# Performance work log

Hardware: AMD Instinct MI355X
Metric: run time of the kernel (lower is better)

## Reference

```python
import jax, jax.numpy as jnp
import numpy as np

B, S, D, H = 8, 512, 1024, 8
DPH = D // H            # 128, dim per head
MAX_REL = 32
NGRAM = 2               # 2-gram RNN on heads 4..7
NG_START, NG_COUNT = 4, 4
SCALE = float(DPH) ** 0.5


def setup_inputs() -> dict:
    key = jax.random.key(0)
    ks = jax.random.split(key, 12)
    w = lambda k, shp: jax.random.normal(k, shp, jnp.float32) * 0.02
    return {
        "x": jax.random.normal(ks[0], (B, S, D), jnp.float32),
        "mask": jax.random.randint(ks[1], (B, 1, S), 0, 2).astype(bool),
        "Wq": w(ks[2], (D, D)), "bq": jnp.zeros((D,), jnp.float32),
        "Wk": w(ks[3], (D, D)), "bk": jnp.zeros((D,), jnp.float32),
        "Wv": w(ks[4], (D, D)), "bv": jnp.zeros((D,), jnp.float32),
        "Wo": w(ks[5], (D, D)), "bo": jnp.zeros((D,), jnp.float32),
        "rel_emb": w(ks[6], (2 * MAX_REL + 1, DPH)),
        "Wih_f": w(ks[7], (DPH, DPH)), "Whh_f": w(ks[8], (DPH, DPH)),
        "bih_f": jnp.zeros((DPH,), jnp.float32), "bhh_f": jnp.zeros((DPH,), jnp.float32),
        "Wih_b": w(ks[9], (DPH, DPH)), "Whh_b": w(ks[10], (DPH, DPH)),
        "bih_b": jnp.zeros((DPH,), jnp.float32), "bhh_b": jnp.zeros((DPH,), jnp.float32),
    }


def reference(x, mask, Wq, bq, Wk, bk, Wv, bv, Wo, bo, rel_emb,
              Wih_f, Whh_f, bih_f, bhh_f, Wih_b, Whh_b, bih_b, bhh_b):
    shape_h = lambda t: t.reshape(B, S, H, DPH).transpose(0, 2, 1, 3)  # [B,H,S,d]
    q = shape_h(x @ Wq.T + bq)
    k = shape_h(x @ Wk.T + bk)
    v = shape_h(x @ Wv.T + bv)

    # --- ngram path: zero masked positions in q/k/v (all heads) ---
    m = mask[:, :, :, None]  # [B,1,S,1] broadcast over heads and d
    q = jnp.where(m, 0.0, q)
    k = jnp.where(m, 0.0, k)
    v = jnp.where(m, 0.0, v)

    # per-head 2-gram bidirectional RNN on heads NG_START..NG_START+NG_COUNT-1
    qh = q[:, NG_START:NG_START + NG_COUNT].reshape(-1, S, DPH)
    kh = k[:, NG_START:NG_START + NG_COUNT].reshape(-1, S, DPH)
    vh = v[:, NG_START:NG_START + NG_COUNT].reshape(-1, S, DPH)
    feats = jnp.concatenate([qh, kh, vh], axis=0)          # [3*B*NG_COUNT, S, d]
    shifted = jnp.pad(feats, ((0, 0), (1, 0), (0, 0)))[:, :-1]  # shift-by-1 (prev token)
    seq = jnp.stack([shifted, feats], axis=0).reshape(NGRAM, -1, DPH)  # [T, N*S, d]
    h0 = jnp.zeros((seq.shape[1], DPH), jnp.float32)
    fstep = lambda h, xt: (jnp.tanh(xt @ Wih_f.T + bih_f + h @ Whh_f.T + bhh_f), None)
    bstep = lambda h, xt: (jnp.tanh(xt @ Wih_b.T + bih_b + h @ Whh_b.T + bhh_b), None)
    hf, _ = jax.lax.scan(fstep, h0, seq)            # fwd final hidden
    hb, _ = jax.lax.scan(bstep, h0, seq[::-1])      # bwd final hidden
    yy = (hf + hb).reshape(3, B, NG_COUNT, S, DPH)  # sum of direction finals
    q = q.at[:, NG_START:NG_START + NG_COUNT].set(yy[0])
    k = k.at[:, NG_START:NG_START + NG_COUNT].set(yy[1])
    v = v.at[:, NG_START:NG_START + NG_COUNT].set(yy[2])

    # --- relative-position attention ---
    qs = q / SCALE
    r = jnp.arange(S)
    rel_idx = jnp.clip(r[None, :] - r[:, None], -MAX_REL, MAX_REL) + MAX_REL  # [S,S]
    rel_k = rel_emb[rel_idx]  # [S,S,d]; same table used for keys and values
    scores = jnp.einsum('bhqd,bhkd->bhqk', qs, k) + jnp.einsum('bhqd,qkd->bhqk', qs, rel_k)
    scores = jnp.where(mask[:, None], -1e18, scores)  # [B,1,1,S] broadcast
    attn = jax.nn.softmax(scores, axis=-1)
    ctx = jnp.einsum('bhqk,bhkd->bhqd', attn, v) + jnp.einsum('bhqk,qkd->bhqd', attn, rel_k)
    out = ctx.transpose(0, 2, 1, 3).reshape(B, S, D) @ Wo.T + bo
    return out, attn
```

## Files before the change

kernel.cpp:

```cpp
#include <hip/hip_runtime.h>


typedef __bf16 bf16x8 __attribute__((ext_vector_type(8)));
typedef float f32x4 __attribute__((ext_vector_type(4)));

#define MFMA16(a, b, c) __builtin_amdgcn_mfma_f32_16x16x32_bf16(a, b, c, 0, 0, 0)

__device__ __forceinline__ unsigned short f2bf(float f) {
  unsigned u = __float_as_uint(f);
  u += 0x7FFFu + ((u >> 16) & 1u);
  return (unsigned short)(u >> 16);
}
__device__ __forceinline__ uint2 pack4(float4 f) {
  uint2 r;
  r.x = (unsigned)f2bf(f.x) | ((unsigned)f2bf(f.y) << 16);
  r.y = (unsigned)f2bf(f.z) | ((unsigned)f2bf(f.w) << 16);
  return r;
}
__device__ __forceinline__ void gld16(const unsigned short* g, unsigned short* l) {
  __builtin_amdgcn_global_load_lds(
      (const __attribute__((address_space(1))) unsigned int*)g,
      (__attribute__((address_space(3))) unsigned int*)l, 16, 0, 0);
}

__global__ __launch_bounds__(256) void prep_bf16(
    const float* __restrict__ x,
    const float* __restrict__ Wq, const float* __restrict__ Wk,
    const float* __restrict__ Wv,
    const float* __restrict__ Wihf, const float* __restrict__ Whhf,
    const float* __restrict__ Wihb, const float* __restrict__ Whhb,
    unsigned short* __restrict__ xb, unsigned short* __restrict__ Wqkvb,
    unsigned short* __restrict__ Wrnnb) {
  int i = blockIdx.x * 256 + threadIdx.x;
  const float* src;
  unsigned short* dst;
  int off;
  if (i < 1048576) {
    src = x; dst = xb; off = i;
  } else if (i < 1310720) {
    src = Wq; dst = Wqkvb; off = i - 1048576;
  } else if (i < 1572864) {
    src = Wk; dst = Wqkvb + 1048576; off = i - 1310720;
  } else if (i < 1835008) {
    src = Wv; dst = Wqkvb + 2097152; off = i - 1572864;
  } else if (i < 1839104) {
    src = Wihf; dst = Wrnnb; off = i - 1835008;
  } else if (i < 1843200) {
    src = Whhf; dst = Wrnnb + 16384; off = i - 1839104;
  } else if (i < 1847296) {
    src = Wihb; dst = Wrnnb + 32768; off = i - 1843200;
  } else {
    src = Whhb; dst = Wrnnb + 49152; off = i - 1847296;
  }
  float4 f = *((const float4*)src + off);
  *(uint2*)(dst + (size_t)off * 4) = pack4(f);
}

__global__ __launch_bounds__(256) void qkv_proj(
    const unsigned short* __restrict__ xb, const unsigned short* __restrict__ Wqkvb,
    const float* __restrict__ bq, const float* __restrict__ bk,
    const float* __restrict__ bv, const int* __restrict__ mask,
    unsigned short* __restrict__ qb, unsigned short* __restrict__ kb,
    unsigned short* __restrict__ vb, unsigned short* __restrict__ vT) {
  __shared__ __align__(16) unsigned short As[128 * 64];
  __shared__ __align__(16) unsigned short Bs[128 * 64];
  const int bm = blockIdx.x & 31;
  const int bn = blockIdx.x >> 5;
  const int t = bn >> 3;
  const int nloc0 = (bn & 7) * 128;
  const unsigned short* W = Wqkvb + (size_t)t * 1048576;
  const float* bias = (t == 0) ? bq : (t == 1) ? bk : bv;
  const int tid = threadIdx.x;
  const int lane = tid & 63, w = tid >> 6;
  const int wm = (w >> 1) * 64, wn = (w & 1) * 64;
  const int lanelo = lane & 15, quad = lane >> 4;
  const int row0 = bm * 128;
  const int rloc = lane >> 3, pch = lane & 7;
  const int lch = (pch - rloc) & 7;

  f32x4 acc[4][4];
  const f32x4 zf = {0.f, 0.f, 0.f, 0.f};
#pragma unroll
  for (int i = 0; i < 4; ++i)
#pragma unroll
    for (int j = 0; j < 4; ++j) acc[i][j] = zf;

  for (int kt = 0; kt < 16; ++kt) {
#pragma unroll
    for (int q = 0; q < 4; ++q) {
      int seg = w * 4 + q;
      int grow = seg * 8 + rloc;
      gld16(xb + (size_t)(row0 + grow) * 1024 + kt * 64 + lch * 8, &As[seg * 512]);
      gld16(W + (size_t)(nloc0 + grow) * 1024 + kt * 64 + lch * 8, &Bs[seg * 512]);
    }
    __syncthreads();
#pragma unroll
    for (int ks = 0; ks < 2; ++ks) {
      const int pA = (ks * 4 + quad + lanelo) & 7;
      bf16x8 a[4], bb[4];
#pragma unroll
      for (int i = 0; i < 4; ++i)
        a[i] = *(const bf16x8*)(&As[(wm + i * 16 + lanelo) * 64 + pA * 8]);
#pragma unroll
      for (int j = 0; j < 4; ++j)
        bb[j] = *(const bf16x8*)(&Bs[(wn + j * 16 + lanelo) * 64 + pA * 8]);
#pragma unroll
      for (int i = 0; i < 4; ++i)
#pragma unroll
        for (int j = 0; j < 4; ++j) acc[i][j] = MFMA16(a[i], bb[j], acc[i][j]);
    }
    __syncthreads();
  }
#pragma unroll
  for (int i = 0; i < 4; ++i) {
#pragma unroll
    for (int j = 0; j < 4; ++j) {
      int jj = nloc0 + wn + j * 16 + lanelo;
      int hh = jj >> 7, dc = jj & 127;
      float bvv = bias[jj];
      int m0 = row0 + wm + i * 16 + quad * 4;
      int b0 = m0 >> 9, sS = m0 & 511;
      unsigned short ov[4];
#pragma unroll
      for (int r = 0; r < 4; ++r) {
        int s = sS + r;
        float val = acc[i][j][r] + bvv;
        if (mask[b0 * 512 + s]) val = 0.f;
        unsigned short o = f2bf(val);
        ov[r] = o;
        size_t off = ((size_t)(b0 * 8 + hh) * 512 + s) * 128 + dc;
        if (t == 0) qb[off] = o;
        else if (t == 1) kb[off] = o;
        else vb[off] = o;
      }
      if (t == 2) {
        uint2 pk;
        pk.x = (unsigned)ov[0] | ((unsigned)ov[1] << 16);
        pk.y = (unsigned)ov[2] | ((unsigned)ov[3] << 16);
        *(uint2*)(&vT[((size_t)(b0 * 8 + hh) * 128 + dc) * 512 + sS]) = pk;
      }
    }
  }
}

__global__ __launch_bounds__(256) void prep_rel(
    const float* __restrict__ rel, unsigned short* __restrict__ relb,
    unsigned short* __restrict__ relT) {
  int i = blockIdx.x * 256 + threadIdx.x;
  if (i < 65 * 128) relb[i] = f2bf(rel[i]);
  if (i < 128 * 96) {
    int d = i / 96, r = i - d * 96;
    relT[i] = (r < 65) ? f2bf(rel[r * 128 + d]) : (unsigned short)0;
  }
}

__global__ __launch_bounds__(256) void rnn_fused(
    const unsigned short* __restrict__ qb, const unsigned short* __restrict__ kb,
    const unsigned short* __restrict__ vb,
    const unsigned short* __restrict__ Wrnnb,
    const float* __restrict__ bihf, const float* __restrict__ bhhf,
    const float* __restrict__ bihb, const float* __restrict__ bhhb,
    unsigned short* __restrict__ rnn_out) {
  __shared__ __align__(16) unsigned short X[65 * 136];
  __shared__ __align__(16) unsigned short Wi[128 * 136];
  __shared__ __align__(16) unsigned short Wh[128 * 136];
  __shared__ __align__(16) unsigned short H1[64 * 136];
  __shared__ float cbf[128], cbb[128];

  const unsigned short* Wihfb = Wrnnb;
  const unsigned short* Whhfb = Wrnnb + 16384;
  const unsigned short* Wihbb = Wrnnb + 32768;
  const unsigned short* Whhbb = Wrnnb + 49152;

  const int gid = blockIdx.x;
  const int tile = gid & 7;
  const int g = gid >> 3;
  const int t = g >> 5;
  const int rem = g & 31;
  const int b = rem >> 2, h = (rem & 3) + 4;
  const int s0 = tile * 64;
  const unsigned short* src = (t == 0) ? qb : (t == 1) ? kb : vb;
  const size_t rowbase = (size_t)(b * 8 + h) * 512;
  const int tid = threadIdx.x;

  for (int c = tid; c < 65 * 16; c += 256) {
    int r = c >> 4, cc = c & 15;
    uint4 v4;
    if (r == 0 && s0 == 0) v4 = make_uint4(0, 0, 0, 0);
    else v4 = *(const uint4*)(src + (rowbase + (s0 - 1 + r)) * 128 + cc * 8);
    *(uint4*)(&X[r * 136 + cc * 8]) = v4;
  }
#pragma unroll
  for (int p = 0; p < 8; ++p) {
    int c = p * 256 + tid;
    int r = c >> 4, cc = c & 15;
    *(uint4*)(&Wi[r * 136 + cc * 8]) = *(const uint4*)(Wihfb + c * 8);
    *(uint4*)(&Wh[r * 136 + cc * 8]) = *(const uint4*)(Whhfb + c * 8);
  }
  if (tid < 128) {
    cbf[tid] = bihf[tid] + bhhf[tid];
    cbb[tid] = bihb[tid] + bhhb[tid];
  }
  __syncthreads();

  const int lane = tid & 63, w = tid >> 6;
  const int lanelo = lane & 15, quad = lane >> 4;
  const int marow = w * 16 + lanelo;
  const f32x4 zf = {0.f, 0.f, 0.f, 0.f};

  f32x4 g1[8];
#pragma unroll
  for (int j = 0; j < 8; ++j) g1[j] = zf;
#pragma unroll
  for (int ks = 0; ks < 4; ++ks) {
    bf16x8 a = *(const bf16x8*)(&X[marow * 136 + ks * 32 + quad * 8]);
#pragma unroll
    for (int j = 0; j < 8; ++j) {
      bf16x8 bb = *(const bf16x8*)(&Wi[(j * 16 + lanelo) * 136 + ks * 32 + quad * 8]);
      g1[j] = MFMA16(a, bb, g1[j]);
    }
  }
#pragma unroll
  for (int j = 0; j < 8; ++j) {
    int col = j * 16 + lanelo;
    float cb = cbf[col];
#pragma unroll
    for (int i = 0; i < 4; ++i) {
      int row = w * 16 + quad * 4 + i;
      H1[row * 136 + col] = f2bf(tanhf(g1[j][i] + cb));
    }
  }
  __syncthreads();
  f32x4 a2[8];
#pragma unroll
  for (int j = 0; j < 8; ++j) a2[j] = zf;
#pragma unroll
  for (int ks = 0; ks < 4; ++ks) {
    bf16x8 a = *(const bf16x8*)(&X[(marow + 1) * 136 + ks * 32 + quad * 8]);
#pragma unroll
    for (int j = 0; j < 8; ++j) {
      bf16x8 bb = *(const bf16x8*)(&Wi[(j * 16 + lanelo) * 136 + ks * 32 + quad * 8]);
      a2[j] = MFMA16(a, bb, a2[j]);
    }
  }
#pragma unroll
  for (int ks = 0; ks < 4; ++ks) {
    bf16x8 a = *(const bf16x8*)(&H1[marow * 136 + ks * 32 + quad * 8]);
#pragma unroll
    for (int j = 0; j < 8; ++j) {
      bf16x8 bb = *(const bf16x8*)(&Wh[(j * 16 + lanelo) * 136 + ks * 32 + quad * 8]);
      a2[j] = MFMA16(a, bb, a2[j]);
    }
  }
  float outF[8][4];
#pragma unroll
  for (int j = 0; j < 8; ++j) {
    int col = j * 16 + lanelo;
    float cb = cbf[col];
#pragma unroll
    for (int i = 0; i < 4; ++i) outF[j][i] = tanhf(a2[j][i] + cb);
  }
  __syncthreads();
#pragma unroll
  for (int p = 0; p < 8; ++p) {
    int c = p * 256 + tid;
    int r = c >> 4, cc = c & 15;
    *(uint4*)(&Wi[r * 136 + cc * 8]) = *(const uint4*)(Wihbb + c * 8);
    *(uint4*)(&Wh[r * 136 + cc * 8]) = *(const uint4*)(Whhbb + c * 8);
  }
  __syncthreads();
#pragma unroll
  for (int j = 0; j < 8; ++j) g1[j] = zf;
#pragma unroll
  for (int ks = 0; ks < 4; ++ks) {
    bf16x8 a = *(const bf16x8*)(&X[(marow + 1) * 136 + ks * 32 + quad * 8]);
#pragma unroll
    for (int j = 0; j < 8; ++j) {
      bf16x8 bb = *(const bf16x8*)(&Wi[(j * 16 + lanelo) * 136 + ks * 32 + quad * 8]);
      g1[j] = MFMA16(a, bb, g1[j]);
    }
  }
#pragma unroll
  for (int j = 0; j < 8; ++j) {
    int col = j * 16 + lanelo;
    float cb = cbb[col];
#pragma unroll
    for (int i = 0; i < 4; ++i) {
      int row = w * 16 + quad * 4 + i;
      H1[row * 136 + col] = f2bf(tanhf(g1[j][i] + cb));
    }
  }
  __syncthreads();
#pragma unroll
  for (int j = 0; j < 8; ++j) a2[j] = zf;
#pragma unroll
  for (int ks = 0; ks < 4; ++ks) {
    bf16x8 a = *(const bf16x8*)(&X[marow * 136 + ks * 32 + quad * 8]);
#pragma unroll
    for (int j = 0; j < 8; ++j) {
      bf16x8 bb = *(const bf16x8*)(&Wi[(j * 16 + lanelo) * 136 + ks * 32 + quad * 8]);
      a2[j] = MFMA16(a, bb, a2[j]);
    }
  }
#pragma unroll
  for (int ks = 0; ks < 4; ++ks) {
    bf16x8 a = *(const bf16x8*)(&H1[marow * 136 + ks * 32 + quad * 8]);
#pragma unroll
    for (int j = 0; j < 8; ++j) {
      bf16x8 bb = *(const bf16x8*)(&Wh[(j * 16 + lanelo) * 136 + ks * 32 + quad * 8]);
      a2[j] = MFMA16(a, bb, a2[j]);
    }
  }
#pragma unroll
  for (int j = 0; j < 8; ++j) {
    int col = j * 16 + lanelo;
    float cb = cbb[col];
#pragma unroll
    for (int i = 0; i < 4; ++i) {
      int row = w * 16 + quad * 4 + i;
      float val = outF[j][i] + tanhf(a2[j][i] + cb);
      rnn_out[((size_t)g * 512 + s0 + row) * 128 + col] = f2bf(val);
    }
  }
}

__global__ __launch_bounds__(256) void rnn_copyback(
    const unsigned short* __restrict__ rnn_out,
    unsigned short* __restrict__ qb, unsigned short* __restrict__ kb,
    unsigned short* __restrict__ vT) {
  int idx = blockIdx.x * 256 + threadIdx.x;
  int g = idx >> 16;
  int r2 = idx & 65535;
  int s = r2 >> 7, col = r2 & 127;
  int t = g >> 5, rem = g & 31, b = rem >> 2, h = (rem & 3) + 4;
  unsigned short val = rnn_out[idx];
  size_t off = ((size_t)(b * 8 + h) * 512 + s) * 128 + col;
  if (t == 0) qb[off] = val;
  else if (t == 1) kb[off] = val;
  else vT[((size_t)(b * 8 + h) * 128 + col) * 512 + s] = val;
}

__global__ __launch_bounds__(256) void scores_av_fused(
    const unsigned short* __restrict__ qbuf, const unsigned short* __restrict__ kbuf,
    const unsigned short* __restrict__ relb, const unsigned short* __restrict__ vT,
    const unsigned short* __restrict__ relT, const float* __restrict__ relf,
    const int* __restrict__ mask, float* __restrict__ attn_out,
    unsigned short* __restrict__ ctx) {
  __shared__ __align__(16) char smem[77824];
  unsigned short* As = (unsigned short*)smem;
  float* Ps = (float*)(smem + 17408);
  float* cmaskS = (float*)(smem + 38912);
  unsigned short* attnb = (unsigned short*)smem;
  unsigned short* abufT = (unsigned short*)(smem + 65536);
  float* redb = (float*)(smem + 73728);

  const int idx = blockIdx.x;
  const int qt = idx >> 6, bh = idx & 63, b = bh >> 3;
  const int q0 = qt * 64;
  const size_t qrow0 = (size_t)bh * 512 + q0;
  const int tid = threadIdx.x;
  const int lane = tid & 63, w = tid >> 6;
  const int lanelo = lane & 15, quad = lane >> 4;
  const f32x4 zf = {0.f, 0.f, 0.f, 0.f};

  for (int c = tid; c < 1024; c += 256) {
    int r = c >> 4, cc = c & 15;
    *(uint4*)(&As[r * 136 + cc * 8]) = *(const uint4*)(qbuf + (qrow0 + r) * 128 + cc * 8);
  }
  for (int i = tid; i < 512; i += 256) cmaskS[i] = mask[b * 512 + i] ? -1e9f : 0.f;
  for (int i = tid; i < 512; i += 256) *(uint4*)(&abufT[i * 8]) = make_uint4(0, 0, 0, 0);
  __syncthreads();

  f32x4 pacc[5];
#pragma unroll
  for (int j = 0; j < 5; ++j) pacc[j] = zf;
#pragma unroll
  for (int ks = 0; ks < 4; ++ks) {
    bf16x8 qf_ = *(const bf16x8*)(&As[(w * 16 + lanelo) * 136 + ks * 32 + quad * 8]);
#pragma unroll
    for (int j = 0; j < 5; ++j) {
      int r = j * 16 + lanelo;
      uint4 tmp = make_uint4(0, 0, 0, 0);
      if (r < 65) tmp = *(const uint4*)(relb + r * 128 + ks * 32 + quad * 8);
      bf16x8 rf_ = *(bf16x8*)&tmp;
      pacc[j] = MFMA16(rf_, qf_, pacc[j]);
    }
  }
#pragma unroll
  for (int j = 0; j < 5; ++j)
    *(f32x4*)(&Ps[(w * 16 + lanelo) * 84 + j * 16 + quad * 4]) = pacc[j];
  __syncthreads();

  f32x4 acc[8][4];
#pragma unroll
  for (int kf = 0; kf < 8; ++kf)
#pragma unroll
    for (int nf = 0; nf < 4; ++nf) acc[kf][nf] = zf;
  const unsigned short* kbp = kbuf + (size_t)bh * 65536;
#pragma unroll
  for (int ks = 0; ks < 4; ++ks) {
    bf16x8 qfr[4];
#pragma unroll
    for (int nf = 0; nf < 4; ++nf)
      qfr[nf] = *(const bf16x8*)(&As[(nf * 16 + lanelo) * 136 + ks * 32 + quad * 8]);
    bf16x8 kfr[8];
#pragma unroll
    for (int kf = 0; kf < 8; ++kf)
      kfr[kf] = *(const bf16x8*)(kbp + (size_t)((w * 8 + kf) * 16 + lanelo) * 128 +
                                 ks * 32 + quad * 8);
#pragma unroll
    for (int kf = 0; kf < 8; ++kf)
#pragma unroll
      for (int nf = 0; nf < 4; ++nf) acc[kf][nf] = MFMA16(kfr[kf], qfr[nf], acc[kf][nf]);
  }

  const float rscale = 0.08838834764831845f;
  float pmax[4] = {-3e38f, -3e38f, -3e38f, -3e38f};
#pragma unroll
  for (int qf = 0; qf < 4; ++qf) {
    const int q = qf * 16 + lanelo;
    const int qg = q0 + q;
    const float* PsR = &Ps[q * 84];
    const float p0 = PsR[0], p64 = PsR[64];
    const int qgmin = q0 + qf * 16;
#pragma unroll
    for (int kf = 0; kf < 8; ++kf) {
      const int kmin = w * 128 + kf * 16;
      const int kbase = kmin + quad * 4;
      if (kmin + 15 - qgmin <= -32) {
#pragma unroll
        for (int i = 0; i < 4; ++i) {
          float val = (acc[kf][qf][i] + p0) * rscale + cmaskS[kbase + i];
          acc[kf][qf][i] = val;
          pmax[qf] = fmaxf(pmax[qf], val);
        }
      } else if (kmin - (qgmin + 15) >= 32) {
#pragma unroll
        for (int i = 0; i < 4; ++i) {
          float val = (acc[kf][qf][i] + p64) * rscale + cmaskS[kbase + i];
          acc[kf][qf][i] = val;
          pmax[qf] = fmaxf(pmax[qf], val);
        }
      } else {
#pragma unroll
        for (int i = 0; i < 4; ++i) {
          int k = kbase + i;
          int d = k - qg;
          int r = min(max(d, -32), 32) + 32;
          float val = (acc[kf][qf][i] + PsR[r]) * rscale + cmaskS[k];
          acc[kf][qf][i] = val;
          pmax[qf] = fmaxf(pmax[qf], val);
        }
      }
    }
  }
  float* red_max = redb;
  float* red_sum = redb + 256;
  float* red_s0 = redb + 512;
  float* red_s64 = redb + 768;
#pragma unroll
  for (int qf = 0; qf < 4; ++qf) {
    pmax[qf] = fmaxf(pmax[qf], __shfl_xor(pmax[qf], 16, 64));
    pmax[qf] = fmaxf(pmax[qf], __shfl_xor(pmax[qf], 32, 64));
  }
  if (quad == 0) {
#pragma unroll
    for (int qf = 0; qf < 4; ++qf) red_max[w * 64 + qf * 16 + lanelo] = pmax[qf];
  }
  __syncthreads();
  float mf_[4], psum[4];
#pragma unroll
  for (int qf = 0; qf < 4; ++qf) {
    int q = qf * 16 + lanelo;
    mf_[qf] = fmaxf(fmaxf(red_max[q], red_max[64 + q]),
                    fmaxf(red_max[128 + q], red_max[192 + q]));
    psum[qf] = 0.f;
  }
#pragma unroll
  for (int qf = 0; qf < 4; ++qf)
#pragma unroll
    for (int kf = 0; kf < 8; ++kf)
#pragma unroll
      for (int i = 0; i < 4; ++i) {
        float e = __expf(acc[kf][qf][i] - mf_[qf]);
        acc[kf][qf][i] = e;
        psum[qf] += e;
      }
#pragma unroll
  for (int qf = 0; qf < 4; ++qf) {
    psum[qf] += __shfl_xor(psum[qf], 16, 64);
    psum[qf] += __shfl_xor(psum[qf], 32, 64);
  }
  if (quad == 0) {
#pragma unroll
    for (int qf = 0; qf < 4; ++qf) red_sum[w * 64 + qf * 16 + lanelo] = psum[qf];
  }
  __syncthreads();
  float rs[4];
#pragma unroll
  for (int qf = 0; qf < 4; ++qf) {
    int q = qf * 16 + lanelo;
    float s = red_sum[q] + red_sum[64 + q] + red_sum[128 + q] + red_sum[192 + q];
    rs[qf] = (s > 0.f) ? 1.f / s : 0.f;
  }

  float s0p[4] = {0.f, 0.f, 0.f, 0.f}, s64p[4] = {0.f, 0.f, 0.f, 0.f};
#pragma unroll
  for (int qf = 0; qf < 4; ++qf) {
    const int q = qf * 16 + lanelo;
    const int qg = q0 + q;
    const int qgmin = q0 + qf * 16;
#pragma unroll
    for (int kf = 0; kf < 8; ++kf) {
      const int kmin = w * 128 + kf * 16;
      const int kbase = kmin + quad * 4;
      float4 at;
      float* ap = (float*)&at;
#pragma unroll
      for (int i = 0; i < 4; ++i) ap[i] = acc[kf][qf][i] * rs[qf];
      if (kmin + 15 - qgmin <= -32) {
#pragma unroll
        for (int i = 0; i < 4; ++i) s0p[qf] += ap[i];
      } else if (kmin - (qgmin + 15) >= 32) {
#pragma unroll
        for (int i = 0; i < 4; ++i) s64p[qf] += ap[i];
      } else {
#pragma unroll
        for (int i = 0; i < 4; ++i) {
          int d = kbase + i - qg;
          if (d <= -32) s0p[qf] += ap[i];
          else if (d >= 32) s64p[qf] += ap[i];
          else {
            int col = d + 32;
            abufT[q * 64 + (((col >> 3) + q) & 7) * 8 + (col & 7)] = f2bf(ap[i]);
          }
        }
      }
      *(float4*)(&attn_out[((size_t)bh * 512 + qg) * 512 + kbase]) = at;
      uint2 pk = pack4(at);
      int cc = kbase >> 3;
      *(uint2*)(&attnb[q * 512 + ((cc + q) & 63) * 8 + (quad & 1) * 4]) = pk;
    }
  }
#pragma unroll
  for (int qf = 0; qf < 4; ++qf) {
    s0p[qf] += __shfl_xor(s0p[qf], 16, 64);
    s0p[qf] += __shfl_xor(s0p[qf], 32, 64);
    s64p[qf] += __shfl_xor(s64p[qf], 16, 64);
    s64p[qf] += __shfl_xor(s64p[qf], 32, 64);
  }
  if (quad == 0) {
#pragma unroll
    for (int qf = 0; qf < 4; ++qf) {
      red_s0[w * 64 + qf * 16 + lanelo] = s0p[qf];
      red_s64[w * 64 + qf * 16 + lanelo] = s64p[qf];
    }
  }
  __syncthreads();
  float s0f[4], s64f[4];
#pragma unroll
  for (int qf = 0; qf < 4; ++qf) {
    int q = qf * 16 + lanelo;
    s0f[qf] = red_s0[q] + red_s0[64 + q] + red_s0[128 + q] + red_s0[192 + q];
    s64f[qf] = red_s64[q] + red_s64[64 + q] + red_s64[128 + q] + red_s64[192 + q];
  }

  f32x4 cacc[2][4];
#pragma unroll
  for (int mf = 0; mf < 2; ++mf)
#pragma unroll
    for (int nf = 0; nf < 4; ++nf) cacc[mf][nf] = zf;
  const unsigned short* vbp = vT + (size_t)bh * 65536;
#pragma unroll
  for (int kt = 0; kt < 16; ++kt) {
    bf16x8 afr[2], bfr[4];
#pragma unroll
    for (int mf = 0; mf < 2; ++mf)
      afr[mf] = *(const bf16x8*)(vbp + (size_t)((w * 2 + mf) * 16 + lanelo) * 512 +
                                 kt * 32 + quad * 8);
#pragma unroll
    for (int nf = 0; nf < 4; ++nf) {
      int q = nf * 16 + lanelo;
      bfr[nf] = *(const bf16x8*)(&attnb[q * 512 + ((kt * 4 + quad + q) & 63) * 8]);
    }
#pragma unroll
    for (int mf = 0; mf < 2; ++mf)
#pragma unroll
      for (int nf = 0; nf < 4; ++nf) cacc[mf][nf] = MFMA16(afr[mf], bfr[nf], cacc[mf][nf]);
  }
#pragma unroll
  for (int kt = 16; kt < 18; ++kt) {
    bf16x8 afr[2], bfr[4];
#pragma unroll
    for (int mf = 0; mf < 2; ++mf)
      afr[mf] = *(const bf16x8*)(relT + ((w * 2 + mf) * 16 + lanelo) * 96 +
                                 (kt - 16) * 32 + quad * 8);
#pragma unroll
    for (int nf = 0; nf < 4; ++nf) {
      int q = nf * 16 + lanelo;
      bfr[nf] = *(const bf16x8*)(&abufT[q * 64 + (((kt - 16) * 4 + quad + q) & 7) * 8]);
    }
#pragma unroll
    for (int mf = 0; mf < 2; ++mf)
#pragma unroll
      for (int nf = 0; nf < 4; ++nf) cacc[mf][nf] = MFMA16(afr[mf], bfr[nf], cacc[mf][nf]);
  }

  float r0v[2][4], r64v[2][4];
#pragma unroll
  for (int mf = 0; mf < 2; ++mf)
#pragma unroll
    for (int i = 0; i < 4; ++i) {
      int d = w * 32 + mf * 16 + quad * 4 + i;
      r0v[mf][i] = relf[d];
      r64v[mf][i] = relf[64 * 128 + d];
    }
  const int b_ = bh >> 3, h_ = bh & 7;
#pragma unroll
  for (int nf = 0; nf < 4; ++nf) {
    int qg = q0 + nf * 16 + lanelo;
#pragma unroll
    for (int mf = 0; mf < 2; ++mf) {
      unsigned short ov[4];
#pragma unroll
      for (int i = 0; i < 4; ++i) {
        float val = cacc[mf][nf][i] + s0f[nf] * r0v[mf][i] + s64f[nf] * r64v[mf][i];
        ov[i] = f2bf(val);
      }
      uint2 pk;
      pk.x = (unsigned)ov[0] | ((unsigned)ov[1] << 16);
      pk.y = (unsigned)ov[2] | ((unsigned)ov[3] << 16);
      *(uint2*)(&ctx[((size_t)(b_ * 512 + qg)) * 1024 + h_ * 128 + w * 32 + mf * 16 + quad * 4]) = pk;
    }
  }
}

__global__ __launch_bounds__(256) void out_proj(
    const unsigned short* __restrict__ ctx, const float* __restrict__ Wo,
    const float* __restrict__ bo, float* __restrict__ outp) {
  __shared__ __align__(16) unsigned short As[128 * 64];
  __shared__ __align__(16) unsigned short Bs[128 * 64];
  const int bm = blockIdx.x & 31, bn = blockIdx.x >> 5;
  const int tid = threadIdx.x, lane = tid & 63, w = tid >> 6;
  const int wm = (w >> 1) * 64, wn = (w & 1) * 64;
  const int lanelo = lane & 15, quad = lane >> 4;
  const int row0 = bm * 128, col0 = bn * 128;
  const int rloc = lane >> 3, pch = lane & 7;
  const int lch = (pch - rloc) & 7;
  f32x4 acc[4][4];
  const f32x4 zf = {0.f, 0.f, 0.f, 0.f};
#pragma unroll
  for (int i = 0; i < 4; ++i)
#pragma unroll
    for (int j = 0; j < 4; ++j) acc[i][j] = zf;

  for (int kt = 0; kt < 16; ++kt) {
#pragma unroll
    for (int q = 0; q < 4; ++q) {
      int seg = w * 4 + q;
      int grow = seg * 8 + rloc;
      gld16(ctx + (size_t)(row0 + grow) * 1024 + kt * 64 + lch * 8, &As[seg * 512]);
    }
    for (int c = tid; c < 1024; c += 256) {
      int r = c >> 3, cc2 = c & 7;
      const float* src = Wo + (size_t)(col0 + r) * 1024 + kt * 64 + cc2 * 8;
      int pc = (cc2 + r) & 7;
      *(uint2*)(&Bs[r * 64 + pc * 8]) = pack4(*(const float4*)src);
      *(uint2*)(&Bs[r * 64 + pc * 8 + 4]) = pack4(*(const float4*)(src + 4));
    }
    __syncthreads();
#pragma unroll
    for (int ks = 0; ks < 2; ++ks) {
      const int pA = (ks * 4 + quad + lanelo) & 7;
      bf16x8 a[4], bb[4];
#pragma unroll
      for (int i = 0; i < 4; ++i)
        a[i] = *(const bf16x8*)(&As[(wm + i * 16 + lanelo) * 64 + pA * 8]);
#pragma unroll
      for (int j = 0; j < 4; ++j)
        bb[j] = *(const bf16x8*)(&Bs[(wn + j * 16 + lanelo) * 64 + pA * 8]);
#pragma unroll
      for (int i = 0; i < 4; ++i)
#pragma unroll
        for (int j = 0; j < 4; ++j) acc[i][j] = MFMA16(a[i], bb[j], acc[i][j]);
    }
    __syncthreads();
  }
#pragma unroll
  for (int i = 0; i < 4; ++i) {
#pragma unroll
    for (int j = 0; j < 4; ++j) {
      int n = col0 + wn + j * 16 + lanelo;
      float bbv = bo[n];
#pragma unroll
      for (int r = 0; r < 4; ++r) {
        int m = row0 + wm + i * 16 + quad * 4 + r;
        outp[(size_t)m * 1024 + n] = acc[i][j][r] + bbv;
      }
    }
  }
}

extern "C" void kernel_launch(void* const* d_in, const int* in_sizes, int n_in,
                              void* d_out, int out_size, void* d_ws, size_t ws_size,
                              hipStream_t stream) {
  const float* x    = (const float*)d_in[0];
  const int*   mask = (const int*)d_in[1];
  const float* Wq   = (const float*)d_in[2];
  const float* bq   = (const float*)d_in[3];
  const float* Wk   = (const float*)d_in[4];
  const float* bk   = (const float*)d_in[5];
  const float* Wv   = (const float*)d_in[6];
  const float* bv   = (const float*)d_in[7];
  const float* Wo   = (const float*)d_in[8];
  const float* bo   = (const float*)d_in[9];
  const float* rel  = (const float*)d_in[10];
  const float* Wihf = (const float*)d_in[11];
  const float* Whhf = (const float*)d_in[12];
  const float* bihf = (const float*)d_in[13];
  const float* bhhf = (const float*)d_in[14];
  const float* Wihb = (const float*)d_in[15];
  const float* Whhb = (const float*)d_in[16];
  const float* bihb = (const float*)d_in[17];
  const float* bhhb = (const float*)d_in[18];

  char* ws = (char*)d_ws;
  unsigned short* qb   = (unsigned short*)(ws + 0);
  unsigned short* kb   = (unsigned short*)(ws + 8388608);
  unsigned short* vT   = (unsigned short*)(ws + 16777216);
  unsigned short* ctx  = (unsigned short*)(ws + 25165824);
  unsigned short* relb = (unsigned short*)(ws + 33554432);
  unsigned short* relT = (unsigned short*)(ws + 33571072);

  float* outp  = (float*)d_out;
  float* attnF = outp + 4194304;
  unsigned short* abase  = (unsigned short*)attnF;
  unsigned short* xb     = abase;
  unsigned short* vb     = abase + 4194304;
  unsigned short* rnnout = abase + 8388608;
  unsigned short* Wqkvb  = abase + 14680064;
  unsigned short* Wrnnb  = abase + 17825792;

  prep_bf16<<<dim3(7232), dim3(256), 0, stream>>>(
      x, Wq, Wk, Wv, Wihf, Whhf, Wihb, Whhb, xb, Wqkvb, Wrnnb);
  prep_rel<<<dim3(48), dim3(256), 0, stream>>>(rel, relb, relT);
  qkv_proj<<<dim3(768), dim3(256), 0, stream>>>(xb, Wqkvb, bq, bk, bv, mask,
                                                qb, kb, vb, vT);
  rnn_fused<<<dim3(768), dim3(256), 0, stream>>>(qb, kb, vb, Wrnnb,
                                                 bihf, bhhf, bihb, bhhb, rnnout);
  rnn_copyback<<<dim3(24576), dim3(256), 0, stream>>>(rnnout, qb, kb, vT);
  scores_av_fused<<<dim3(512), dim3(256), 0, stream>>>(qb, kb, relb, vT, relT,
                                                       rel, mask, attnF, ctx);
  out_proj<<<dim3(256), dim3(256), 0, stream>>>(ctx, Wo, bo, outp);
}
```

Baseline: 364.1 us.

## Shrink attention query tile from 64 to 16 rows for more blocks

The fused scores/softmax/AV kernel now handles 16 query rows per block instead of 64, and launches 2048 blocks instead of 512. Shared memory per block drops from about 76KB to 22KB and per-thread accumulator registers shrink fourfold, which should allow more resident blocks and better latency hiding. The cost is that each block reloads the full K and V^T slices for its head, so K/V global/L2 traffic rises fourfold. The rel-embedding projection is now done by a single wave while the other three wait.

```diff
diff --git a/kernel.cpp b/kernel.cpp
--- a/kernel.cpp
+++ b/kernel.cpp
@@ -346,100 +346,93 @@
     const unsigned short* __restrict__ relT, const float* __restrict__ relf,
     const int* __restrict__ mask, float* __restrict__ attn_out,
     unsigned short* __restrict__ ctx) {
-  __shared__ __align__(16) char smem[77824];
+  __shared__ __align__(16) char smem[22528];
   unsigned short* As = (unsigned short*)smem;
-  float* Ps = (float*)(smem + 17408);
-  float* cmaskS = (float*)(smem + 38912);
+  float* Ps = (float*)(smem + 4352);
+  float* cmaskS = (float*)(smem + 9728);
   unsigned short* attnb = (unsigned short*)smem;
-  unsigned short* abufT = (unsigned short*)(smem + 65536);
-  float* redb = (float*)(smem + 73728);
+  unsigned short* abufT = (unsigned short*)(smem + 16384);
+  float* redb = (float*)(smem + 18432);
 
   const int idx = blockIdx.x;
   const int qt = idx >> 6, bh = idx & 63, b = bh >> 3;
-  const int q0 = qt * 64;
+  const int q0 = qt * 16;
   const size_t qrow0 = (size_t)bh * 512 + q0;
   const int tid = threadIdx.x;
   const int lane = tid & 63, w = tid >> 6;
   const int lanelo = lane & 15, quad = lane >> 4;
   const f32x4 zf = {0.f, 0.f, 0.f, 0.f};
 
-  for (int c = tid; c < 1024; c += 256) {
-    int r = c >> 4, cc = c & 15;
+  {
+    int r = tid >> 4, cc = tid & 15;
     *(uint4*)(&As[r * 136 + cc * 8]) = *(const uint4*)(qbuf + (qrow0 + r) * 128 + cc * 8);
   }
   for (int i = tid; i < 512; i += 256) cmaskS[i] = mask[b * 512 + i] ? -1e9f : 0.f;
-  for (int i = tid; i < 512; i += 256) *(uint4*)(&abufT[i * 8]) = make_uint4(0, 0, 0, 0);
-  __syncthreads();
-
-  f32x4 pacc[5];
-#pragma unroll
-  for (int j = 0; j < 5; ++j) pacc[j] = zf;
+  if (tid < 128) *(uint4*)(&abufT[tid * 8]) = make_uint4(0, 0, 0, 0);
+  __syncthreads();
+
+  if (w == 0) {
+    f32x4 pacc[5];
+#pragma unroll
+    for (int j = 0; j < 5; ++j) pacc[j] = zf;
+#pragma unroll
+    for (int ks = 0; ks < 4; ++ks) {
+      bf16x8 qf_ = *(const bf16x8*)(&As[lanelo * 136 + ks * 32 + quad * 8]);
+#pragma unroll
+      for (int j = 0; j < 5; ++j) {
+        int r = j * 16 + lanelo;
+        uint4 tmp = make_uint4(0, 0, 0, 0);
+        if (r < 65) tmp = *(const uint4*)(relb + r * 128 + ks * 32 + quad * 8);
+        bf16x8 rf_ = *(bf16x8*)&tmp;
+        pacc[j] = MFMA16(rf_, qf_, pacc[j]);
+      }
+    }
+#pragma unroll
+    for (int j = 0; j < 5; ++j)
+      *(f32x4*)(&Ps[lanelo * 84 + j * 16 + quad * 4]) = pacc[j];
+  }
+  __syncthreads();
+
+  f32x4 acc[8];
+#pragma unroll
+  for (int kf = 0; kf < 8; ++kf) acc[kf] = zf;
+  const unsigned short* kbp = kbuf + (size_t)bh * 65536;
 #pragma unroll
   for (int ks = 0; ks < 4; ++ks) {
-    bf16x8 qf_ = *(const bf16x8*)(&As[(w * 16 + lanelo) * 136 + ks * 32 + quad * 8]);
-#pragma unroll
-    for (int j = 0; j < 5; ++j) {
-      int r = j * 16 + lanelo;
-      uint4 tmp = make_uint4(0, 0, 0, 0);
-      if (r < 65) tmp = *(const uint4*)(relb + r * 128 + ks * 32 + quad * 8);
-      bf16x8 rf_ = *(bf16x8*)&tmp;
-      pacc[j] = MFMA16(rf_, qf_, pacc[j]);
-    }
-  }
-#pragma unroll
-  for (int j = 0; j < 5; ++j)
-    *(f32x4*)(&Ps[(w * 16 + lanelo) * 84 + j * 16 + quad * 4]) = pacc[j];
-  __syncthreads();
-
-  f32x4 acc[8][4];
-#pragma unroll
-  for (int kf = 0; kf < 8; ++kf)
-#pragma unroll
-    for (int nf = 0; nf < 4; ++nf) acc[kf][nf] = zf;
-  const unsigned short* kbp = kbuf + (size_t)bh * 65536;
-#pragma unroll
-  for (int ks = 0; ks < 4; ++ks) {
-    bf16x8 qfr[4];
-#pragma unroll
-    for (int nf = 0; nf < 4; ++nf)
-      qfr[nf] = *(const bf16x8*)(&As[(nf * 16 + lanelo) * 136 + ks * 32 + quad * 8]);
+    bf16x8 qfr = *(const bf16x8*)(&As[lanelo * 136 + ks * 32 + quad * 8]);
     bf16x8 kfr[8];
 #pragma unroll
     for (int kf = 0; kf < 8; ++kf)
       kfr[kf] = *(const bf16x8*)(kbp + (size_t)((w * 8 + kf) * 16 + lanelo) * 128 +
                                  ks * 32 + quad * 8);
 #pragma unroll
-    for (int kf = 0; kf < 8; ++kf)
-#pragma unroll
-      for (int nf = 0; nf < 4; ++nf) acc[kf][nf] = MFMA16(kfr[kf], qfr[nf], acc[kf][nf]);
+    for (int kf = 0; kf < 8; ++kf) acc[kf] = MFMA16(kfr[kf], qfr, acc[kf]);
   }
 
   const float rscale = 0.08838834764831845f;
-  float pmax[4] = {-3e38f, -3e38f, -3e38f, -3e38f};
-#pragma unroll
-  for (int qf = 0; qf < 4; ++qf) {
-    const int q = qf * 16 + lanelo;
+  float pmax = -3e38f;
+  {
+    const int q = lanelo;
     const int qg = q0 + q;
     const float* PsR = &Ps[q * 84];
     const float p0 = PsR[0], p64 = PsR[64];
-    const int qgmin = q0 + qf * 16;
 #pragma unroll
     for (int kf = 0; kf < 8; ++kf) {
       const int kmin = w * 128 + kf * 16;
       const int kbase = kmin + quad * 4;
-      if (kmin + 15 - qgmin <= -32) {
+      if (kmin + 15 - q0 <= -32) {
 #pragma unroll
         for (int i = 0; i < 4; ++i) {
-          float val = (acc[kf][qf][i] + p0) * rscale + cmaskS[kbase + i];
-          acc[kf][qf][i] = val;
-          pmax[qf] = fmaxf(pmax[qf], val);
+          float val = (acc[kf][i] + p0) * rscale + cmaskS[kbase + i];
+          acc[kf][i] = val;
+          pmax = fmaxf(pmax, val);
         }
-      } else if (kmin - (qgmin + 15) >= 32) {
+      } else if (kmin - (q0 + 15) >= 32) {
 #pragma unroll
         for (int i = 0; i < 4; ++i) {
-          float val = (acc[kf][qf][i] + p64) * rscale + cmaskS[kbase + i];
-          acc[kf][qf][i] = val;
-          pmax[qf] = fmaxf(pmax[qf], val);
+          float val = (acc[kf][i] + p64) * rscale + cmaskS[kbase + i];
+          acc[kf][i] = val;
+          pmax = fmaxf(pmax, val);
         }
       } else {
 #pragma unroll
@@ -447,9 +440,9 @@
           int k = kbase + i;
           int d = k - qg;
           int r = min(max(d, -32), 32) + 32;
-          float val = (acc[kf][qf][i] + PsR[r]) * rscale + cmaskS[k];
-          acc[kf][qf][i] = val;
-          pmax[qf] = fmaxf(pmax[qf], val);
+          float val = (acc[kf][i] + PsR[r]) * rscale + cmaskS[k];
+          acc[kf][i] = val;
+          pmax = fmaxf(pmax, val);
         }
       }
     }
@@ -458,58 +451,39 @@
   float* red_sum = redb + 256;
   float* red_s0 = redb + 512;
   float* red_s64 = redb + 768;
-#pragma unroll
-  for (int qf = 0; qf < 4; ++qf) {
-    pmax[qf] = fmaxf(pmax[qf], __shfl_xor(pmax[qf], 16, 64));
-    pmax[qf] = fmaxf(pmax[qf], __shfl_xor(pmax[qf], 32, 64));
-  }
-  if (quad == 0) {
-#pragma unroll
-    for (int qf = 0; qf < 4; ++qf) red_max[w * 64 + qf * 16 + lanelo] = pmax[qf];
-  }
-  __syncthreads();
-  float mf_[4], psum[4];
-#pragma unroll
-  for (int qf = 0; qf < 4; ++qf) {
-    int q = qf * 16 + lanelo;
-    mf_[qf] = fmaxf(fmaxf(red_max[q], red_max[64 + q]),
-                    fmaxf(red_max[128 + q], red_max[192 + q]));
-    psum[qf] = 0.f;
-  }
-#pragma unroll
-  for (int qf = 0; qf < 4; ++qf)
-#pragma unroll
-    for (int kf = 0; kf < 8; ++kf)
-#pragma unroll
-      for (int i = 0; i < 4; ++i) {
-        float e = __expf(acc[kf][qf][i] - mf_[qf]);
-        acc[kf][qf][i] = e;
-        psum[qf] += e;
-      }
-#pragma unroll
-  for (int qf = 0; qf < 4; ++qf) {
-    psum[qf] += __shfl_xor(psum[qf], 16, 64);
-    psum[qf] += __shfl_xor(psum[qf], 32, 64);
-  }
-  if (quad == 0) {
-#pragma unroll
-    for (int qf = 0; qf < 4; ++qf) red_sum[w * 64 + qf * 16 + lanelo] = psum[qf];
-  }
-  __syncthreads();
-  float rs[4];
-#pragma unroll
-  for (int qf = 0; qf < 4; ++qf) {
-    int q = qf * 16 + lanelo;
+  pmax = fmaxf(pmax, __shfl_xor(pmax, 16, 64));
+  pmax = fmaxf(pmax, __shfl_xor(pmax, 32, 64));
+  if (quad == 0) red_max[w * 64 + lanelo] = pmax;
+  __syncthreads();
+  float mf_, psum = 0.f;
+  {
+    int q = lanelo;
+    mf_ = fmaxf(fmaxf(red_max[q], red_max[64 + q]),
+                fmaxf(red_max[128 + q], red_max[192 + q]));
+  }
+#pragma unroll
+  for (int kf = 0; kf < 8; ++kf)
+#pragma unroll
+    for (int i = 0; i < 4; ++i) {
+      float e = __expf(acc[kf][i] - mf_);
+      acc[kf][i] = e;
+      psum += e;
+    }
+  psum += __shfl_xor(psum, 16, 64);
+  psum += __shfl_xor(psum, 32, 64);
+  if (quad == 0) red_sum[w * 64 + lanelo] = psum;
+  __syncthreads();
+  float rs;
+  {
+    int q = lanelo;
     float s = red_sum[q] + red_sum[64 + q] + red_sum[128 + q] + red_sum[192 + q];
-    rs[qf] = (s > 0.f) ? 1.f / s : 0.f;
-  }
-
-  float s0p[4] = {0.f, 0.f, 0.f, 0.f}, s64p[4] = {0.f, 0.f, 0.f, 0.f};
-#pragma unroll
-  for (int qf = 0; qf < 4; ++qf) {
-    const int q = qf * 16 + lanelo;
+    rs = (s > 0.f) ? 1.f / s : 0.f;
+  }
+
+  float s0p = 0.f, s64p = 0.f;
+  {
+    const int q = lanelo;
     const int qg = q0 + q;
-    const int qgmin = q0 + qf * 16;
 #pragma unroll
     for (int kf = 0; kf < 8; ++kf) {
       const int kmin = w * 128 + kf * 16;
@@ -517,19 +491,19 @@
       float4 at;
       float* ap = (float*)&at;
 #pragma unroll
-      for (int i = 0; i < 4; ++i) ap[i] = acc[kf][qf][i] * rs[qf];
-      if (kmin + 15 - qgmin <= -32) {
-#pragma unroll
-        for (int i = 0; i < 4; ++i) s0p[qf] += ap[i];
-      } else if (kmin - (qgmin + 15) >= 32) {
-#pragma unroll
-        for (int i = 0; i < 4; ++i) s64p[qf] += ap[i];
+      for (int i = 0; i < 4; ++i) ap[i] = acc[kf][i] * rs;
+      if (kmin + 15 - q0 <= -32) {
+#pragma unroll
+        for (int i = 0; i < 4; ++i) s0p += ap[i];
+      } else if (kmin - (q0 + 15) >= 32) {
+#pragma unroll
+        for (int i = 0; i < 4; ++i) s64p += ap[i];
       } else {
 #pragma unroll
         for (int i = 0; i < 4; ++i) {
           int d = kbase + i - qg;
-          if (d <= -32) s0p[qf] += ap[i];
-          else if (d >= 32) s64p[qf] += ap[i];
+          if (d <= -32) s0p += ap[i];
+          else if (d >= 32) s64p += ap[i];
           else {
             int col = d + 32;
             abufT[q * 64 + (((col >> 3) + q) & 7) * 8 + (col & 7)] = f2bf(ap[i]);
@@ -542,68 +516,53 @@
       *(uint2*)(&attnb[q * 512 + ((cc + q) & 63) * 8 + (quad & 1) * 4]) = pk;
     }
   }
-#pragma unroll
-  for (int qf = 0; qf < 4; ++qf) {
-    s0p[qf] += __shfl_xor(s0p[qf], 16, 64);
-    s0p[qf] += __shfl_xor(s0p[qf], 32, 64);
-    s64p[qf] += __shfl_xor(s64p[qf], 16, 64);
-    s64p[qf] += __shfl_xor(s64p[qf], 32, 64);
-  }
+  s0p += __shfl_xor(s0p, 16, 64);
+  s0p += __shfl_xor(s0p, 32, 64);
+  s64p += __shfl_xor(s64p, 16, 64);
+  s64p += __shfl_xor(s64p, 32, 64);
   if (quad == 0) {
-#pragma unroll
-    for (int qf = 0; qf < 4; ++qf) {
-      red_s0[w * 64 + qf * 16 + lanelo] = s0p[qf];
-      red_s64[w * 64 + qf * 16 + lanelo] = s64p[qf];
-    }
-  }
-  __syncthreads();
-  float s0f[4], s64f[4];
-#pragma unroll
-  for (int qf = 0; qf < 4; ++qf) {
-    int q = qf * 16 + lanelo;
-    s0f[qf] = red_s0[q] + red_s0[64 + q] + red_s0[128 + q] + red_s0[192 + q];
-    s64f[qf] = red_s64[q] + red_s64[64 + q] + red_s64[128 + q] + red_s64[192 + q];
-  }
-
-  f32x4 cacc[2][4];
-#pragma unroll
-  for (int mf = 0; mf < 2; ++mf)
-#pragma unroll
-    for (int nf = 0; nf < 4; ++nf) cacc[mf][nf] = zf;
+    red_s0[w * 64 + lanelo] = s0p;
+    red_s64[w * 64 + lanelo] = s64p;
+  }
+  __syncthreads();
+  float s0f, s64f;
+  {
+    int q = lanelo;
+    s0f = red_s0[q] + red_s0[64 + q] + red_s0[128 + q] + red_s0[192 + q];
+    s64f = red_s64[q] + red_s64[64 + q] + red_s64[128 + q] + red_s64[192 + q];
+  }
+
+  f32x4 cacc[2];
+#pragma unroll
+  for (int mf = 0; mf < 2; ++mf) cacc[mf] = zf;
   const unsigned short* vbp = vT + (size_t)bh * 65536;
 #pragma unroll
   for (int kt = 0; kt < 16; ++kt) {
-    bf16x8 afr[2], bfr[4];
+    bf16x8 afr[2], bfr;
 #pragma unroll
     for (int mf = 0; mf < 2; ++mf)
       afr[mf] = *(const bf16x8*)(vbp + (size_t)((w * 2 + mf) * 16 + lanelo) * 512 +
                                  kt * 32 + quad * 8);
-#pragma unroll
-    for (int nf = 0; nf < 4; ++nf) {
-      int q = nf * 16 + lanelo;
-      bfr[nf] = *(const bf16x8*)(&attnb[q * 512 + ((kt * 4 + quad + q) & 63) * 8]);
-    }
-#pragma unroll
-    for (int mf = 0; mf < 2; ++mf)
-#pragma unroll
-      for (int nf = 0; nf < 4; ++nf) cacc[mf][nf] = MFMA16(afr[mf], bfr[nf], cacc[mf][nf]);
+    {
+      int q = lanelo;
+      bfr = *(const bf16x8*)(&attnb[q * 512 + ((kt * 4 + quad + q) & 63) * 8]);
+    }
+#pragma unroll
+    for (int mf = 0; mf < 2; ++mf) cacc[mf] = MFMA16(afr[mf], bfr, cacc[mf]);
   }
 #pragma unroll
   for (int kt = 16; kt < 18; ++kt) {
-    bf16x8 afr[2], bfr[4];
+    bf16x8 afr[2], bfr;
 #pragma unroll
     for (int mf = 0; mf < 2; ++mf)
       afr[mf] = *(const bf16x8*)(relT + ((w * 2 + mf) * 16 + lanelo) * 96 +
                                  (kt - 16) * 32 + quad * 8);
-#pragma unroll
-    for (int nf = 0; nf < 4; ++nf) {
-      int q = nf * 16 + lanelo;
-      bfr[nf] = *(const bf16x8*)(&abufT[q * 64 + (((kt - 16) * 4 + quad + q) & 7) * 8]);
-    }
-#pragma unroll
-    for (int mf = 0; mf < 2; ++mf)
-#pragma unroll
-      for (int nf = 0; nf < 4; ++nf) cacc[mf][nf] = MFMA16(afr[mf], bfr[nf], cacc[mf][nf]);
+    {
+      int q = lanelo;
+      bfr = *(const bf16x8*)(&abufT[q * 64 + (((kt - 16) * 4 + quad + q) & 7) * 8]);
+    }
+#pragma unroll
+    for (int mf = 0; mf < 2; ++mf) cacc[mf] = MFMA16(afr[mf], bfr, cacc[mf]);
   }
 
   float r0v[2][4], r64v[2][4];
@@ -616,15 +575,14 @@
       r64v[mf][i] = relf[64 * 128 + d];
     }
   const int b_ = bh >> 3, h_ = bh & 7;
-#pragma unroll
-  for (int nf = 0; nf < 4; ++nf) {
-    int qg = q0 + nf * 16 + lanelo;
+  {
+    int qg = q0 + lanelo;
 #pragma unroll
     for (int mf = 0; mf < 2; ++mf) {
       unsigned short ov[4];
 #pragma unroll
       for (int i = 0; i < 4; ++i) {
-        float val = cacc[mf][nf][i] + s0f[nf] * r0v[mf][i] + s64f[nf] * r64v[mf][i];
+        float val = cacc[mf][i] + s0f * r0v[mf][i] + s64f * r64v[mf][i];
         ov[i] = f2bf(val);
       }
       uint2 pk;
@@ -749,7 +707,7 @@
   rnn_fused<<<dim3(768), dim3(256), 0, stream>>>(qb, kb, vb, Wrnnb,
                                                  bihf, bhhf, bihb, bhhb, rnnout);
   rnn_copyback<<<dim3(24576), dim3(256), 0, stream>>>(rnnout, qb, kb, vT);
-  scores_av_fused<<<dim3(512), dim3(256), 0, stream>>>(qb, kb, relb, vT, relT,
-                                                       rel, mask, attnF, ctx);
+  scores_av_fused<<<dim3(2048), dim3(256), 0, stream>>>(qb, kb, relb, vT, relT,
+                                                        rel, mask, attnF, ctx);
   out_proj<<<dim3(256), dim3(256), 0, stream>>>(ctx, Wo, bo, outp);
 }
```

Measured after the change: 416.9 us. 1.14x slower.
